# Kernel tuning notes

Measured on AMD Instinct MI355X. Metric: run time of the kernel, lower is better.

Reference implementation:

```python
import jax, jax.numpy as jnp
import numpy as np

T = 20.0
SCALE = 0.3


def setup_inputs() -> dict:
    key = jax.random.key(0)
    k1, k2, k3 = jax.random.split(key, 3)
    N, C = 65536, 1000
    outputs1 = jax.random.normal(k1, (N, C), dtype=jnp.float32)
    outputs2 = jax.random.normal(k2, (N, C), dtype=jnp.float32)
    targets = jax.random.randint(k3, (N,), 0, C, dtype=jnp.int64)
    return {"outputs1": outputs1, "outputs2": outputs2, "targets": targets}


def reference(outputs1, outputs2, targets):
    # temperature softmax over classes
    p1 = jax.nn.softmax(outputs1 / T, axis=1)  # [N, C]
    p2 = jax.nn.softmax(outputs2 / T, axis=1)  # [N, C]
    # mean-center each row
    vx = p1 - jnp.mean(p1, axis=1, keepdims=True)
    vy = p2 - jnp.mean(p2, axis=1, keepdims=True)
    # per-row Pearson correlation
    num = jnp.sum(vx * vy, axis=1)
    den = jnp.sqrt(jnp.sum(vx * vx, axis=1)) * jnp.sqrt(jnp.sum(vy * vy, axis=1))
    cost = num / den  # [N]
    return jnp.mean(SCALE * cost)
```

## Files before the change

kernel.cpp:

```cpp
#include <hip/hip_runtime.h>


#define N_ROWS   65536
#define N_C      1000
#define NBLOCKS  2048
#define WPB      4
#define RPW      8

__device__ __forceinline__ void gload16(const float* g, float* s) {
    __builtin_amdgcn_global_load_lds(
        (const __attribute__((address_space(1))) void*)g,
        (__attribute__((address_space(3))) void*)s, 16, 0, 0);
}

__device__ __forceinline__ void stage_row(const float* __restrict__ o1,
                                          const float* __restrict__ o2,
                                          long row, float* dst, int lane) {
    const float* r1 = o1 + row * (long)N_C;
    const float* r2 = o2 + row * (long)N_C;
    const int l4 = lane * 4;
    gload16(r1 + l4,       dst);
    gload16(r1 + 256 + l4, dst + 256);
    gload16(r1 + 512 + l4, dst + 512);
    gload16(r2 + l4,       dst + 1024);
    gload16(r2 + 256 + l4, dst + 1280);
    gload16(r2 + 512 + l4, dst + 1536);
    bool tail_ok = (lane < 58) || (row + 1 < (long)N_ROWS);
    if (tail_ok) {
        gload16(r1 + 768 + l4, dst + 768);
        gload16(r2 + 768 + l4, dst + 1792);
    }
}

__device__ __forceinline__ double row_cost(const float* buf, int lane) {
    const float4* A = reinterpret_cast<const float4*>(buf);
    const float4* B = reinterpret_cast<const float4*>(buf + 1024);
    constexpr float INV_T = 1.0f / 20.0f;
    float sx = 0.f, sy = 0.f, sxx = 0.f, syy = 0.f, sxy = 0.f;
    #pragma unroll
    for (int k = 0; k < 4; ++k) {
        float4 a = A[k * 64 + lane];
        float4 b = B[k * 64 + lane];
        const bool ok = (k < 3) || (lane < 58);
        float av[4] = {a.x, a.y, a.z, a.w};
        float bv[4] = {b.x, b.y, b.z, b.w};
        #pragma unroll
        for (int e = 0; e < 4; ++e) {
            float va = ok ? av[e] : 0.0f;
            float vb = ok ? bv[e] : 0.0f;
            float x = __expf(va * INV_T) - 1.0f;
            float y = __expf(vb * INV_T) - 1.0f;
            sx += x;  sy += y;
            sxx = fmaf(x, x, sxx);
            syy = fmaf(y, y, syy);
            sxy = fmaf(x, y, sxy);
        }
    }
    #pragma unroll
    for (int off = 32; off; off >>= 1) {
        sx  += __shfl_xor(sx,  off, 64);
        sy  += __shfl_xor(sy,  off, 64);
        sxx += __shfl_xor(sxx, off, 64);
        syy += __shfl_xor(syy, off, 64);
        sxy += __shfl_xor(sxy, off, 64);
    }
    constexpr double invC = 1.0 / (double)N_C;
    double dx = (double)sx, dy = (double)sy;
    double num = (double)sxy - dx * dy * invC;
    double vx  = (double)sxx - dx * dx * invC;
    double vy  = (double)syy - dy * dy * invC;
    return num / sqrt(vx * vy);
}

__global__ __launch_bounds__(256) void div2_stage1(
        const float* __restrict__ o1, const float* __restrict__ o2,
        double* __restrict__ ws) {
    __shared__ float lds[WPB][2][2048];
    const int wave = threadIdx.x >> 6;
    const int lane = threadIdx.x & 63;
    const int gw   = blockIdx.x * WPB + wave;
    const long r0  = (long)gw * RPW;

    float* buf0 = &lds[wave][0][0];
    float* buf1 = &lds[wave][1][0];

    stage_row(o1, o2, r0, buf0, lane);

    double acc = 0.0;
    #pragma unroll 1
    for (int p = 0; p < RPW; ++p) {
        float* cur = (p & 1) ? buf1 : buf0;
        float* nxt = (p & 1) ? buf0 : buf1;
        if (p + 1 < RPW) {
            stage_row(o1, o2, r0 + p + 1, nxt, lane);
            asm volatile("s_waitcnt vmcnt(8)" ::: "memory");
        } else {
            asm volatile("s_waitcnt vmcnt(0)" ::: "memory");
        }
        acc += row_cost(cur, lane);
    }

    __syncthreads();
    double* dred = reinterpret_cast<double*>(&lds[0][0][0]);
    if (lane == 0) dred[wave] = acc;
    __syncthreads();
    if (threadIdx.x == 0)
        ws[blockIdx.x] = dred[0] + dred[1] + dred[2] + dred[3];
}

__global__ __launch_bounds__(256) void div2_stage2(
        const double* __restrict__ ws, int n, float* __restrict__ out) {
    double s = 0.0;
    for (int i = threadIdx.x; i < n; i += 256) s += ws[i];
    #pragma unroll
    for (int off = 32; off; off >>= 1) s += __shfl_xor(s, off, 64);
    __shared__ double lds[4];
    const int wave = threadIdx.x >> 6;
    const int lane = threadIdx.x & 63;
    if (lane == 0) lds[wave] = s;
    __syncthreads();
    if (threadIdx.x == 0) {
        double t = lds[0] + lds[1] + lds[2] + lds[3];
        out[0] = (float)(t * (0.3 / (double)N_ROWS));
    }
}

extern "C" void kernel_launch(void* const* d_in, const int* in_sizes, int n_in,
                              void* d_out, int out_size, void* d_ws, size_t ws_size,
                              hipStream_t stream) {
    const float* o1 = (const float*)d_in[0];
    const float* o2 = (const float*)d_in[1];
    float* out = (float*)d_out;
    double* ws = (double*)d_ws;

    div2_stage1<<<NBLOCKS, 256, 0, stream>>>(o1, o2, ws);
    div2_stage2<<<1, 256, 0, stream>>>(ws, NBLOCKS, out);
}
```

Measured before the change: 104.0 us.

## Fuse final reduction via last-block atomic counter and enlarge rows per wave

Replaces the separate second-stage reduction kernel with a last-block-done pattern: each block writes its partial sum, increments an atomic counter, and the final block reduces all partials and writes the output. A memset of the counter is added on the stream. The grid shrinks to 512 blocks with 32 rows per wave, which cuts per-block overhead but may reduce occupancy and latency hiding. The tail load is also made unconditional by redirecting out-of-range lanes to a safe address, so the vmcnt waits stay uniform.

```diff
diff --git a/kernel.cpp b/kernel.cpp
--- a/kernel.cpp
+++ b/kernel.cpp
@@ -1,11 +1,11 @@
 #include <hip/hip_runtime.h>
 
 
-#define N_ROWS   65536
-#define N_C      1000
-#define NBLOCKS  2048
-#define WPB      4
-#define RPW      8
+#define N_ROWS  65536
+#define N_C     1000
+#define NBLOCKS 512
+#define WPB     4
+#define RPW     32
 
 __device__ __forceinline__ void gload16(const float* g, float* s) {
     __builtin_amdgcn_global_load_lds(
@@ -13,11 +13,9 @@
         (__attribute__((address_space(3))) void*)s, 16, 0, 0);
 }
 
-__device__ __forceinline__ void stage_row(const float* __restrict__ o1,
-                                          const float* __restrict__ o2,
-                                          long row, float* dst, int lane) {
-    const float* r1 = o1 + row * (long)N_C;
-    const float* r2 = o2 + row * (long)N_C;
+__device__ __forceinline__ void stage_row(const float* __restrict__ r1,
+                                          const float* __restrict__ r2,
+                                          bool final_row, float* dst, int lane) {
     const int l4 = lane * 4;
     gload16(r1 + l4,       dst);
     gload16(r1 + 256 + l4, dst + 256);
@@ -25,11 +23,11 @@
     gload16(r2 + l4,       dst + 1024);
     gload16(r2 + 256 + l4, dst + 1280);
     gload16(r2 + 512 + l4, dst + 1536);
-    bool tail_ok = (lane < 58) || (row + 1 < (long)N_ROWS);
-    if (tail_ok) {
-        gload16(r1 + 768 + l4, dst + 768);
-        gload16(r2 + 768 + l4, dst + 1792);
-    }
+    const float* a3 = r1 + 768 + l4;
+    const float* b3 = r2 + 768 + l4;
+    if (final_row && lane >= 58) { a3 = r1; b3 = r2; }
+    gload16(a3, dst + 768);
+    gload16(b3, dst + 1792);
 }
 
 __device__ __forceinline__ double row_cost(const float* buf, int lane) {
@@ -72,10 +70,14 @@
     return num / sqrt(vx * vy);
 }
 
-__global__ __launch_bounds__(256) void div2_stage1(
+__global__ __launch_bounds__(256) void div2_fused(
         const float* __restrict__ o1, const float* __restrict__ o2,
-        double* __restrict__ ws) {
+        double* __restrict__ ws, unsigned int* __restrict__ cnt,
+        float* __restrict__ out) {
     __shared__ float lds[WPB][2][2048];
+    __shared__ double dred[WPB];
+    __shared__ int slast;
+
     const int wave = threadIdx.x >> 6;
     const int lane = threadIdx.x & 63;
     const int gw   = blockIdx.x * WPB + wave;
@@ -84,7 +86,9 @@
     float* buf0 = &lds[wave][0][0];
     float* buf1 = &lds[wave][1][0];
 
-    stage_row(o1, o2, r0, buf0, lane);
+    const float* row1 = o1 + r0 * (long)N_C;
+    const float* row2 = o2 + r0 * (long)N_C;
+    stage_row(row1, row2, r0 == (long)N_ROWS - 1, buf0, lane);
 
     double acc = 0.0;
     #pragma unroll 1
@@ -92,7 +96,9 @@
         float* cur = (p & 1) ? buf1 : buf0;
         float* nxt = (p & 1) ? buf0 : buf1;
         if (p + 1 < RPW) {
-            stage_row(o1, o2, r0 + p + 1, nxt, lane);
+            long nr = r0 + p + 1;
+            stage_row(o1 + nr * (long)N_C, o2 + nr * (long)N_C,
+                      nr == (long)N_ROWS - 1, nxt, lane);
             asm volatile("s_waitcnt vmcnt(8)" ::: "memory");
         } else {
             asm volatile("s_waitcnt vmcnt(0)" ::: "memory");
@@ -100,28 +106,31 @@
         acc += row_cost(cur, lane);
     }
 
-    __syncthreads();
-    double* dred = reinterpret_cast<double*>(&lds[0][0][0]);
     if (lane == 0) dred[wave] = acc;
     __syncthreads();
-    if (threadIdx.x == 0)
-        ws[blockIdx.x] = dred[0] + dred[1] + dred[2] + dred[3];
-}
+    if (threadIdx.x == 0) {
+        double part = dred[0] + dred[1] + dred[2] + dred[3];
+        ws[blockIdx.x] = part;
+        unsigned int old = __hip_atomic_fetch_add(cnt, 1u, __ATOMIC_ACQ_REL,
+                                                  __HIP_MEMORY_SCOPE_AGENT);
+        slast = (old == NBLOCKS - 1);
+    }
+    __syncthreads();
 
-__global__ __launch_bounds__(256) void div2_stage2(
-        const double* __restrict__ ws, int n, float* __restrict__ out) {
-    double s = 0.0;
-    for (int i = threadIdx.x; i < n; i += 256) s += ws[i];
-    #pragma unroll
-    for (int off = 32; off; off >>= 1) s += __shfl_xor(s, off, 64);
-    __shared__ double lds[4];
-    const int wave = threadIdx.x >> 6;
-    const int lane = threadIdx.x & 63;
-    if (lane == 0) lds[wave] = s;
-    __syncthreads();
-    if (threadIdx.x == 0) {
-        double t = lds[0] + lds[1] + lds[2] + lds[3];
-        out[0] = (float)(t * (0.3 / (double)N_ROWS));
+    if (slast) {
+        const int t = threadIdx.x;
+        double s = 0.0;
+        #pragma unroll
+        for (int i = 0; i < NBLOCKS / 256; ++i)
+            s += __hip_atomic_load(&ws[t + i * 256], __ATOMIC_RELAXED,
+                                   __HIP_MEMORY_SCOPE_AGENT);
+        #pragma unroll
+        for (int off = 32; off; off >>= 1) s += __shfl_xor(s, off, 64);
+        if (lane == 0) dred[wave] = s;
+        __syncthreads();
+        if (t == 0)
+            out[0] = (float)((dred[0] + dred[1] + dred[2] + dred[3]) *
+                             (0.3 / (double)N_ROWS));
     }
 }
 
@@ -132,7 +141,9 @@
     const float* o2 = (const float*)d_in[1];
     float* out = (float*)d_out;
     double* ws = (double*)d_ws;
+    unsigned int* cnt = (unsigned int*)((char*)d_ws + NBLOCKS * sizeof(double));
 
-    div2_stage1<<<NBLOCKS, 256, 0, stream>>>(o1, o2, ws);
-    div2_stage2<<<1, 256, 0, stream>>>(ws, NBLOCKS, out);
+    hipMemsetAsync((void*)cnt, 0, sizeof(unsigned int), stream);
+
+    div2_fused<<<NBLOCKS, 256, 0, stream>>>(o1, o2, ws, cnt, out);
 }
```

Result: slower. 120.6 us (+15.9%).
